# Performance work log

Measured on AMD Instinct MI355X. Metric: run time of the kernel, lower is better.

## Reference

```python
import jax, jax.numpy as jnp
import numpy as np
import math

B, S, D = 4, 4096, 2048
H = 16
DH = D // H  # 128
EPS = 1e-5


def _layer_norm(x, g, b):
    m = jnp.mean(x, axis=-1, keepdims=True)
    v = jnp.mean(jnp.square(x - m), axis=-1, keepdims=True)
    return (x - m) * jax.lax.rsqrt(v + EPS) * g + b


def setup_inputs() -> dict:
    key = jax.random.key(0)
    ks = jax.random.split(key, 12)
    s = 0.02
    return {
        "X": jax.random.normal(ks[0], (B, S, D), dtype=jnp.float32),
        "Wq": jax.random.normal(ks[1], (D, D), dtype=jnp.float32) * s,
        "bq": jnp.zeros((D,), dtype=jnp.float32),
        "Wk": jax.random.normal(ks[2], (D, D), dtype=jnp.float32) * s,
        "bk": jnp.zeros((D,), dtype=jnp.float32),
        "Wv": jax.random.normal(ks[3], (D, D), dtype=jnp.float32) * s,
        "bv": jnp.zeros((D,), dtype=jnp.float32),
        "g1": jnp.ones((D,), dtype=jnp.float32),
        "beta1": jnp.zeros((D,), dtype=jnp.float32),
        "W1": jax.random.normal(ks[4], (D, D), dtype=jnp.float32) * s,
        "b1": jnp.zeros((D,), dtype=jnp.float32),
        "W2": jax.random.normal(ks[5], (D, D), dtype=jnp.float32) * s,
        "b2": jnp.zeros((D,), dtype=jnp.float32),
        "g2": jnp.ones((D,), dtype=jnp.float32),
        "beta2": jnp.zeros((D,), dtype=jnp.float32),
    }


def reference(X, Wq, bq, Wk, bk, Wv, bv, g1, beta1, W1, b1, W2, b2, g2, beta2):
    # --- MultiHeadSelfAttention (faithful: .view, so attention is over HEADS per token) ---
    q = (X @ Wq + bq).reshape(B, S, H, DH)
    k = (X @ Wk + bk).reshape(B, S, H, DH)
    v = (X @ Wv + bv).reshape(B, S, H, DH)
    # [B, S, H, H] scores: heads attend to heads within the same position
    att = jnp.einsum('bshd,bstd->bsht', q, k) / math.sqrt(DH)
    att = jax.nn.softmax(att, axis=-1)
    y = jnp.einsum('bsht,bstd->bshd', att, v).reshape(B, S, D)
    # --- residual + LN1 ---
    X1 = _layer_norm(X + y, g1, beta1)
    # --- FeedForward: D -> D -> D with exact GELU ---
    h = jax.nn.gelu(X1 @ W1 + b1, approximate=False)
    y2 = h @ W2 + b2
    # --- residual + LN2 ---
    return _layer_norm(X1 + y2, g2, beta2)
```

## Files before the change

kernel.cpp:

```cpp
#include <hip/hip_runtime.h>
#include <math.h>

#define DM 2048
#define NT 16384
#define KD 2048
#define ND 2048

typedef __bf16 bf16x8 __attribute__((ext_vector_type(8)));
typedef float  f32x4  __attribute__((ext_vector_type(4)));

__device__ __forceinline__ void gld_lds16(const void* g, void* l) {
  __builtin_amdgcn_global_load_lds(
      (const __attribute__((address_space(1))) unsigned int*)g,
      (__attribute__((address_space(3))) unsigned int*)l, 16, 0, 0);
}

__global__ __launch_bounds__(256) void k_cast(const float* __restrict__ x,
                                              __bf16* __restrict__ y) {
  const size_t i = ((size_t)blockIdx.x * 256 + threadIdx.x) * 8;
  const float4 a = *(const float4*)(x + i);
  const float4 b = *(const float4*)(x + i + 4);
  bf16x8 o;
  o[0]=(__bf16)a.x; o[1]=(__bf16)a.y; o[2]=(__bf16)a.z; o[3]=(__bf16)a.w;
  o[4]=(__bf16)b.x; o[5]=(__bf16)b.y; o[6]=(__bf16)b.z; o[7]=(__bf16)b.w;
  *(bf16x8*)(y + i) = o;
}

__global__ __launch_bounds__(256) void k_transpose(const float* __restrict__ W,
                                                   __bf16* __restrict__ Wt) {
  __shared__ float t[32][33];
  const int tx = threadIdx.x, ty = threadIdx.y;
  const int n  = blockIdx.x * 32 + tx;
  const int k0 = blockIdx.y * 32;
  #pragma unroll
  for (int j = 0; j < 32; j += 8) t[ty + j][tx] = W[(size_t)(k0 + ty + j) * ND + n];
  __syncthreads();
  const int kk = k0 + tx;
  const int n0 = blockIdx.x * 32;
  #pragma unroll
  for (int j = 0; j < 32; j += 8)
    Wt[(size_t)(n0 + ty + j) * KD + kk] = (__bf16)t[tx][ty + j];
}

__global__ __launch_bounds__(256, 2) void k_gemm(
    const __bf16* __restrict__ A, const __bf16* __restrict__ Bt,
    const float* __restrict__ bias, const int mode,
    __bf16* __restrict__ outb, const float* __restrict__ resf,
    const __bf16* __restrict__ resb, float* __restrict__ outf) {
  __shared__ __bf16 As[128 * 32];
  __shared__ __bf16 Bs[128 * 32];
  const int tid  = threadIdx.x;
  const int wave = tid >> 6, lane = tid & 63;
  const int quad = lane >> 4, r16 = lane & 15;
  const int m0 = blockIdx.x * 128, n0 = blockIdx.y * 128;
  const int wm = (wave >> 1) * 64, wn = (wave & 1) * 64;

  const int srow = tid >> 2;
  const int scol = (tid & 3) * 8;
  const __bf16* Ap0 = A  + (size_t)(m0 + srow) * KD + scol;
  const __bf16* Ap1 = A  + (size_t)(m0 + 64 + srow) * KD + scol;
  const __bf16* Bp0 = Bt + (size_t)(n0 + srow) * KD + scol;
  const __bf16* Bp1 = Bt + (size_t)(n0 + 64 + srow) * KD + scol;
  __bf16* AsW0 = &As[wave * 512];
  __bf16* AsW1 = &As[2048 + wave * 512];
  __bf16* BsW0 = &Bs[wave * 512];
  __bf16* BsW1 = &Bs[2048 + wave * 512];

  f32x4 acc[4][4] = {};

  for (int k0 = 0; k0 < KD; k0 += 32) {
    gld_lds16(Ap0 + k0, AsW0);
    gld_lds16(Ap1 + k0, AsW1);
    gld_lds16(Bp0 + k0, BsW0);
    gld_lds16(Bp1 + k0, BsW1);
    __syncthreads();
    bf16x8 af[4], bfr[4];
    #pragma unroll
    for (int mi = 0; mi < 4; mi++)
      af[mi] = *(const bf16x8*)&As[(wm + mi * 16 + r16) * 32 + quad * 8];
    #pragma unroll
    for (int ni = 0; ni < 4; ni++)
      bfr[ni] = *(const bf16x8*)&Bs[(wn + ni * 16 + r16) * 32 + quad * 8];
    #pragma unroll
    for (int mi = 0; mi < 4; mi++)
      #pragma unroll
      for (int ni = 0; ni < 4; ni++)
        acc[mi][ni] = __builtin_amdgcn_mfma_f32_16x16x32_bf16(af[mi], bfr[ni], acc[mi][ni], 0, 0, 0);
    __syncthreads();
  }

  #pragma unroll
  for (int ni = 0; ni < 4; ni++) {
    const int gn = n0 + wn + ni * 16 + r16;
    const float bv = bias[gn];
    #pragma unroll
    for (int mi = 0; mi < 4; mi++) {
      const int gm = m0 + wm + mi * 16 + quad * 4;
      if (mode == 0) {
        #pragma unroll
        for (int r = 0; r < 4; r++)
          outb[(size_t)(gm + r) * ND + gn] = (__bf16)(acc[mi][ni][r] + bv);
      } else if (mode == 1) {
        #pragma unroll
        for (int r = 0; r < 4; r++) {
          float v = acc[mi][ni][r] + bv;
          float gel = 0.5f * v * (1.0f + erff(v * 0.70710678118654752f));
          outb[(size_t)(gm + r) * ND + gn] = (__bf16)gel;
        }
      } else if (mode == 2) {
        #pragma unroll
        for (int r = 0; r < 4; r++) {
          const size_t o = (size_t)(gm + r) * ND + gn;
          outf[o] = acc[mi][ni][r] + bv + resf[o];
        }
      } else {
        #pragma unroll
        for (int r = 0; r < 4; r++) {
          const size_t o = (size_t)(gm + r) * ND + gn;
          outf[o] = acc[mi][ni][r] + bv + (float)resb[o];
        }
      }
    }
  }
}

__global__ __launch_bounds__(256) void k_attn_ln1(
    const __bf16* __restrict__ Q, const __bf16* __restrict__ Kq,
    const __bf16* __restrict__ V, const float* __restrict__ X,
    const float* __restrict__ g1, const float* __restrict__ be1,
    float* __restrict__ X1, __bf16* __restrict__ X1b, const int use_f32) {
  __shared__ float qs[16 * 132];
  __shared__ float ks[16 * 132];
  __shared__ float vs[16 * 132];
  __shared__ float p[256];
  __shared__ float red[8];
  const int tid = threadIdx.x;
  const size_t base = (size_t)blockIdx.x * DM;
  const int e0 = tid * 8;

  {
    const int row = e0 >> 7, c0 = e0 & 127;
    bf16x8 qv = *(const bf16x8*)(Q + base + e0);
    bf16x8 kv = *(const bf16x8*)(Kq + base + e0);
    bf16x8 vv = *(const bf16x8*)(V + base + e0);
    #pragma unroll
    for (int j = 0; j < 8; j++) {
      qs[row * 132 + c0 + j] = (float)qv[j];
      ks[row * 132 + c0 + j] = (float)kv[j];
      vs[row * 132 + c0 + j] = (float)vv[j];
    }
  }
  __syncthreads();

  {
    const int h = tid >> 4, t = tid & 15;
    const float* qp = &qs[h * 132];
    const float* kp = &ks[t * 132];
    float s = 0.f;
    #pragma unroll
    for (int d = 0; d < 128; d++) s += qp[d] * kp[d];
    s *= 0.08838834764831845f;
    float mx = s;
    #pragma unroll
    for (int off = 8; off; off >>= 1) mx = fmaxf(mx, __shfl_xor(mx, off, 16));
    const float e = expf(s - mx);
    float sum = e;
    #pragma unroll
    for (int off = 8; off; off >>= 1) sum += __shfl_xor(sum, off, 16);
    p[tid] = e / sum;
  }
  __syncthreads();

  float zloc[8];
  float zs = 0.f, zq = 0.f;
  {
    const float4 x1 = *(const float4*)(X + base + e0);
    const float4 x2 = *(const float4*)(X + base + e0 + 4);
    const float xr[8] = {x1.x, x1.y, x1.z, x1.w, x2.x, x2.y, x2.z, x2.w};
    const int hh = e0 >> 7;
    const int d0 = e0 & 127;
    const float* pp = &p[hh * 16];
    #pragma unroll
    for (int j = 0; j < 8; j++) {
      float y = 0.f;
      #pragma unroll
      for (int t2 = 0; t2 < 16; t2++) y += pp[t2] * vs[t2 * 132 + d0 + j];
      const float z = xr[j] + y;
      zloc[j] = z; zs += z; zq += z * z;
    }
  }
  #pragma unroll
  for (int off = 32; off; off >>= 1) {
    zs += __shfl_xor(zs, off, 64);
    zq += __shfl_xor(zq, off, 64);
  }
  const int wave = tid >> 6, lane = tid & 63;
  if (lane == 0) { red[wave] = zs; red[4 + wave] = zq; }
  __syncthreads();
  zs = red[0] + red[1] + red[2] + red[3];
  zq = red[4] + red[5] + red[6] + red[7];
  const float mean = zs * (1.f / DM);
  const float var = zq * (1.f / DM) - mean * mean;
  const float rstd = rsqrtf(var + 1e-5f);
  {
    float o[8];
    #pragma unroll
    for (int j = 0; j < 8; j++)
      o[j] = (zloc[j] - mean) * rstd * g1[e0 + j] + be1[e0 + j];
    if (use_f32) {
      *(float4*)(X1 + base + e0)     = make_float4(o[0], o[1], o[2], o[3]);
      *(float4*)(X1 + base + e0 + 4) = make_float4(o[4], o[5], o[6], o[7]);
    }
    bf16x8 ob;
    #pragma unroll
    for (int j = 0; j < 8; j++) ob[j] = (__bf16)o[j];
    *(bf16x8*)(X1b + base + e0) = ob;
  }
}

__global__ __launch_bounds__(256) void k_ln2(const float* __restrict__ Z,
                                             const float* __restrict__ g,
                                             const float* __restrict__ be,
                                             float* __restrict__ out) {
  __shared__ float red[8];
  const int tid = threadIdx.x;
  const size_t base = (size_t)blockIdx.x * DM;
  const int e0 = tid * 8;
  const float4 a = *(const float4*)(Z + base + e0);
  const float4 b = *(const float4*)(Z + base + e0 + 4);
  float z[8] = {a.x, a.y, a.z, a.w, b.x, b.y, b.z, b.w};
  float zs = 0.f, zq = 0.f;
  #pragma unroll
  for (int j = 0; j < 8; j++) { zs += z[j]; zq += z[j] * z[j]; }
  #pragma unroll
  for (int off = 32; off; off >>= 1) {
    zs += __shfl_xor(zs, off, 64);
    zq += __shfl_xor(zq, off, 64);
  }
  const int wave = tid >> 6, lane = tid & 63;
  if (lane == 0) { red[wave] = zs; red[4 + wave] = zq; }
  __syncthreads();
  zs = red[0] + red[1] + red[2] + red[3];
  zq = red[4] + red[5] + red[6] + red[7];
  const float mean = zs * (1.f / DM);
  const float var = zq * (1.f / DM) - mean * mean;
  const float rstd = rsqrtf(var + 1e-5f);
  float o[8];
  #pragma unroll
  for (int j = 0; j < 8; j++)
    o[j] = (z[j] - mean) * rstd * g[e0 + j] + be[e0 + j];
  *(float4*)(out + base + e0)     = make_float4(o[0], o[1], o[2], o[3]);
  *(float4*)(out + base + e0 + 4) = make_float4(o[4], o[5], o[6], o[7]);
}

extern "C" void kernel_launch(void* const* d_in, const int* in_sizes, int n_in,
                              void* d_out, int out_size, void* d_ws, size_t ws_size,
                              hipStream_t stream) {
  const float* X   = (const float*)d_in[0];
  const float* Wq  = (const float*)d_in[1];
  const float* bq  = (const float*)d_in[2];
  const float* Wk  = (const float*)d_in[3];
  const float* bk  = (const float*)d_in[4];
  const float* Wv  = (const float*)d_in[5];
  const float* bv  = (const float*)d_in[6];
  const float* g1  = (const float*)d_in[7];
  const float* be1 = (const float*)d_in[8];
  const float* W1  = (const float*)d_in[9];
  const float* b1  = (const float*)d_in[10];
  const float* W2  = (const float*)d_in[11];
  const float* b2  = (const float*)d_in[12];
  const float* g2  = (const float*)d_in[13];
  const float* be2 = (const float*)d_in[14];
  float* out = (float*)d_out;

  char* ws = (char*)d_ws;
  size_t off = 0;
  auto alloc = [&](size_t b) -> char* {
    char* p = ws + off;
    off += (b + 255) & ~(size_t)255;
    return p;
  };
  const size_t EL = (size_t)NT * DM;
  __bf16* Xb  = (__bf16*)alloc(EL * 2);
  __bf16* Wqt = (__bf16*)alloc((size_t)ND * KD * 2);
  __bf16* Wkt = (__bf16*)alloc((size_t)ND * KD * 2);
  __bf16* Wvt = (__bf16*)alloc((size_t)ND * KD * 2);
  __bf16* W1t = (__bf16*)alloc((size_t)ND * KD * 2);
  __bf16* W2t = (__bf16*)alloc((size_t)ND * KD * 2);
  __bf16* Qb  = (__bf16*)alloc(EL * 2);
  __bf16* Kb  = (__bf16*)alloc(EL * 2);
  __bf16* Vb  = (__bf16*)alloc(EL * 2);
  __bf16* X1b = (__bf16*)alloc(EL * 2);
  const int use_f32 = (ws_size >= off + EL * 4) ? 1 : 0;
  float* X1 = nullptr;
  if (use_f32) X1 = (float*)alloc(EL * 4);
  __bf16* Hb = Xb;
  float*  Z  = (float*)Qb;

  k_cast<<<dim3(NT * DM / 2048), dim3(256), 0, stream>>>(X, Xb);
  dim3 tb(32, 8), tg(64, 64);
  k_transpose<<<tg, tb, 0, stream>>>(Wq, Wqt);
  k_transpose<<<tg, tb, 0, stream>>>(Wk, Wkt);
  k_transpose<<<tg, tb, 0, stream>>>(Wv, Wvt);
  k_transpose<<<tg, tb, 0, stream>>>(W1, W1t);
  k_transpose<<<tg, tb, 0, stream>>>(W2, W2t);
  dim3 gg(NT / 128, ND / 128);
  k_gemm<<<gg, dim3(256), 0, stream>>>(Xb, Wqt, bq, 0, Qb, nullptr, nullptr, nullptr);
  k_gemm<<<gg, dim3(256), 0, stream>>>(Xb, Wkt, bk, 0, Kb, nullptr, nullptr, nullptr);
  k_gemm<<<gg, dim3(256), 0, stream>>>(Xb, Wvt, bv, 0, Vb, nullptr, nullptr, nullptr);
  k_attn_ln1<<<dim3(NT), dim3(256), 0, stream>>>(Qb, Kb, Vb, X, g1, be1, X1, X1b, use_f32);
  k_gemm<<<gg, dim3(256), 0, stream>>>(X1b, W1t, b1, 1, Hb, nullptr, nullptr, nullptr);
  k_gemm<<<gg, dim3(256), 0, stream>>>(Hb, W2t, b2, use_f32 ? 2 : 3, nullptr, X1, X1b, Z);
  k_ln2<<<dim3(NT), dim3(256), 0, stream>>>(Z, g2, be2, out);
}
```

Baseline: 1.412 ms.

## Fuse QKV projections into one GEMM with LDS-staged vectorized epilogue

Concatenates the transposed Wq/Wk/Wv into one 6144-wide weight and the three biases into one buffer, so Q, K and V come from a single GEMM launch instead of three. The attention kernel reads an interleaved QKV row. The GEMM now uses a 1D grid with N-fastest tile ordering, which should improve reuse of A tiles in cache. The bf16-output epilogues stage results through LDS so each thread writes 16-byte vectors instead of scattered 2-byte stores. The costs are one extra small bias-copy kernel and a larger QKV workspace buffer.

```diff
diff --git a/kernel.cpp b/kernel.cpp
--- a/kernel.cpp
+++ b/kernel.cpp
@@ -4,7 +4,6 @@
 #define DM 2048
 #define NT 16384
 #define KD 2048
-#define ND 2048
 
 typedef __bf16 bf16x8 __attribute__((ext_vector_type(8)));
 typedef float  f32x4  __attribute__((ext_vector_type(4)));
@@ -33,7 +32,7 @@
   const int n  = blockIdx.x * 32 + tx;
   const int k0 = blockIdx.y * 32;
   #pragma unroll
-  for (int j = 0; j < 32; j += 8) t[ty + j][tx] = W[(size_t)(k0 + ty + j) * ND + n];
+  for (int j = 0; j < 32; j += 8) t[ty + j][tx] = W[(size_t)(k0 + ty + j) * DM + n];
   __syncthreads();
   const int kk = k0 + tx;
   const int n0 = blockIdx.x * 32;
@@ -42,9 +41,18 @@
     Wt[(size_t)(n0 + ty + j) * KD + kk] = (__bf16)t[tx][ty + j];
 }
 
+__global__ __launch_bounds__(256) void k_bias3(const float* __restrict__ a,
+                                               const float* __restrict__ b,
+                                               const float* __restrict__ c,
+                                               float* __restrict__ o) {
+  const int i = blockIdx.x * 256 + threadIdx.x;
+  o[i] = (i < 2048) ? a[i] : ((i < 4096) ? b[i - 2048] : c[i - 4096]);
+}
+
 __global__ __launch_bounds__(256, 2) void k_gemm(
     const __bf16* __restrict__ A, const __bf16* __restrict__ Bt,
-    const float* __restrict__ bias, const int mode,
+    const float* __restrict__ bias, const int mode, const int ntile_n,
+    const int NS,
     __bf16* __restrict__ outb, const float* __restrict__ resf,
     const __bf16* __restrict__ resb, float* __restrict__ outf) {
   __shared__ __bf16 As[128 * 32];
@@ -52,7 +60,9 @@
   const int tid  = threadIdx.x;
   const int wave = tid >> 6, lane = tid & 63;
   const int quad = lane >> 4, r16 = lane & 15;
-  const int m0 = blockIdx.x * 128, n0 = blockIdx.y * 128;
+  const int bid = blockIdx.x;
+  const int m0 = (bid / ntile_n) * 128;
+  const int n0 = (bid % ntile_n) * 128;
   const int wm = (wave >> 1) * 64, wn = (wave & 1) * 64;
 
   const int srow = tid >> 2;
@@ -89,44 +99,61 @@
     __syncthreads();
   }
 
-  #pragma unroll
-  for (int ni = 0; ni < 4; ni++) {
-    const int gn = n0 + wn + ni * 16 + r16;
-    const float bv = bias[gn];
-    #pragma unroll
-    for (int mi = 0; mi < 4; mi++) {
-      const int gm = m0 + wm + mi * 16 + quad * 4;
-      if (mode == 0) {
+  if (mode <= 1) {
+    __bf16* eb = (wave < 2) ? &As[wave * 2048] : &Bs[(wave - 2) * 2048];
+    #pragma unroll
+    for (int half = 0; half < 2; half++) {
+      #pragma unroll
+      for (int nj = 0; nj < 2; nj++) {
+        const int ni = half * 2 + nj;
+        const int gn = n0 + wn + ni * 16 + r16;
+        const float bv = bias[gn];
         #pragma unroll
-        for (int r = 0; r < 4; r++)
-          outb[(size_t)(gm + r) * ND + gn] = (__bf16)(acc[mi][ni][r] + bv);
-      } else if (mode == 1) {
-        #pragma unroll
-        for (int r = 0; r < 4; r++) {
-          float v = acc[mi][ni][r] + bv;
-          float gel = 0.5f * v * (1.0f + erff(v * 0.70710678118654752f));
-          outb[(size_t)(gm + r) * ND + gn] = (__bf16)gel;
-        }
-      } else if (mode == 2) {
-        #pragma unroll
-        for (int r = 0; r < 4; r++) {
-          const size_t o = (size_t)(gm + r) * ND + gn;
-          outf[o] = acc[mi][ni][r] + bv + resf[o];
-        }
-      } else {
-        #pragma unroll
-        for (int r = 0; r < 4; r++) {
-          const size_t o = (size_t)(gm + r) * ND + gn;
-          outf[o] = acc[mi][ni][r] + bv + (float)resb[o];
+        for (int mi = 0; mi < 4; mi++) {
+          #pragma unroll
+          for (int r = 0; r < 4; r++) {
+            float v = acc[mi][ni][r] + bv;
+            if (mode == 1) v = 0.5f * v * (1.0f + erff(v * 0.70710678118654752f));
+            eb[(mi * 16 + quad * 4 + r) * 32 + nj * 16 + r16] = (__bf16)v;
+          }
         }
       }
+      #pragma unroll
+      for (int rd = 0; rd < 4; rd++) {
+        const int row = rd * 16 + (lane >> 2);
+        const int c0 = (lane & 3) * 8;
+        bf16x8 vv = *(const bf16x8*)&eb[row * 32 + c0];
+        *(bf16x8*)(outb + (size_t)(m0 + wm + row) * NS + n0 + wn + half * 32 + c0) = vv;
+      }
+    }
+  } else {
+    #pragma unroll
+    for (int ni = 0; ni < 4; ni++) {
+      const int gn = n0 + wn + ni * 16 + r16;
+      const float bv = bias[gn];
+      #pragma unroll
+      for (int mi = 0; mi < 4; mi++) {
+        const int gm = m0 + wm + mi * 16 + quad * 4;
+        if (mode == 2) {
+          #pragma unroll
+          for (int r = 0; r < 4; r++) {
+            const size_t o = (size_t)(gm + r) * NS + gn;
+            outf[o] = acc[mi][ni][r] + bv + resf[o];
+          }
+        } else {
+          #pragma unroll
+          for (int r = 0; r < 4; r++) {
+            const size_t o = (size_t)(gm + r) * NS + gn;
+            outf[o] = acc[mi][ni][r] + bv + (float)resb[o];
+          }
+        }
+      }
     }
   }
 }
 
 __global__ __launch_bounds__(256) void k_attn_ln1(
-    const __bf16* __restrict__ Q, const __bf16* __restrict__ Kq,
-    const __bf16* __restrict__ V, const float* __restrict__ X,
+    const __bf16* __restrict__ QKV, const float* __restrict__ X,
     const float* __restrict__ g1, const float* __restrict__ be1,
     float* __restrict__ X1, __bf16* __restrict__ X1b, const int use_f32) {
   __shared__ float qs[16 * 132];
@@ -135,14 +162,15 @@
   __shared__ float p[256];
   __shared__ float red[8];
   const int tid = threadIdx.x;
-  const size_t base = (size_t)blockIdx.x * DM;
+  const size_t qbase = (size_t)blockIdx.x * 6144;
+  const size_t base  = (size_t)blockIdx.x * DM;
   const int e0 = tid * 8;
 
   {
     const int row = e0 >> 7, c0 = e0 & 127;
-    bf16x8 qv = *(const bf16x8*)(Q + base + e0);
-    bf16x8 kv = *(const bf16x8*)(Kq + base + e0);
-    bf16x8 vv = *(const bf16x8*)(V + base + e0);
+    bf16x8 qv = *(const bf16x8*)(QKV + qbase + e0);
+    bf16x8 kv = *(const bf16x8*)(QKV + qbase + 2048 + e0);
+    bf16x8 vv = *(const bf16x8*)(QKV + qbase + 4096 + e0);
     #pragma unroll
     for (int j = 0; j < 8; j++) {
       qs[row * 132 + c0 + j] = (float)qv[j];
@@ -280,36 +308,36 @@
     off += (b + 255) & ~(size_t)255;
     return p;
   };
-  const size_t EL = (size_t)NT * DM;
-  __bf16* Xb  = (__bf16*)alloc(EL * 2);
-  __bf16* Wqt = (__bf16*)alloc((size_t)ND * KD * 2);
-  __bf16* Wkt = (__bf16*)alloc((size_t)ND * KD * 2);
-  __bf16* Wvt = (__bf16*)alloc((size_t)ND * KD * 2);
-  __bf16* W1t = (__bf16*)alloc((size_t)ND * KD * 2);
-  __bf16* W2t = (__bf16*)alloc((size_t)ND * KD * 2);
-  __bf16* Qb  = (__bf16*)alloc(EL * 2);
-  __bf16* Kb  = (__bf16*)alloc(EL * 2);
-  __bf16* Vb  = (__bf16*)alloc(EL * 2);
-  __bf16* X1b = (__bf16*)alloc(EL * 2);
+  const size_t EL  = (size_t)NT * DM;
+  const size_t EL3 = (size_t)NT * 6144;
+  __bf16* Xb    = (__bf16*)alloc(EL * 2);
+  __bf16* Wqkvt = (__bf16*)alloc((size_t)6144 * KD * 2);
+  __bf16* W1t   = (__bf16*)alloc((size_t)DM * KD * 2);
+  __bf16* W2t   = (__bf16*)alloc((size_t)DM * KD * 2);
+  float*  b3    = (float*)alloc(6144 * 4);
+  __bf16* QKVb  = (__bf16*)alloc(EL3 * 2);
+  __bf16* X1b   = (__bf16*)alloc(EL * 2);
   const int use_f32 = (ws_size >= off + EL * 4) ? 1 : 0;
   float* X1 = nullptr;
   if (use_f32) X1 = (float*)alloc(EL * 4);
   __bf16* Hb = Xb;
-  float*  Z  = (float*)Qb;
+  float*  Z  = (float*)QKVb;
 
   k_cast<<<dim3(NT * DM / 2048), dim3(256), 0, stream>>>(X, Xb);
   dim3 tb(32, 8), tg(64, 64);
-  k_transpose<<<tg, tb, 0, stream>>>(Wq, Wqt);
-  k_transpose<<<tg, tb, 0, stream>>>(Wk, Wkt);
-  k_transpose<<<tg, tb, 0, stream>>>(Wv, Wvt);
+  k_transpose<<<tg, tb, 0, stream>>>(Wq, Wqkvt);
+  k_transpose<<<tg, tb, 0, stream>>>(Wk, Wqkvt + (size_t)2048 * KD);
+  k_transpose<<<tg, tb, 0, stream>>>(Wv, Wqkvt + (size_t)4096 * KD);
   k_transpose<<<tg, tb, 0, stream>>>(W1, W1t);
   k_transpose<<<tg, tb, 0, stream>>>(W2, W2t);
-  dim3 gg(NT / 128, ND / 128);
-  k_gemm<<<gg, dim3(256), 0, stream>>>(Xb, Wqt, bq, 0, Qb, nullptr, nullptr, nullptr);
-  k_gemm<<<gg, dim3(256), 0, stream>>>(Xb, Wkt, bk, 0, Kb, nullptr, nullptr, nullptr);
-  k_gemm<<<gg, dim3(256), 0, stream>>>(Xb, Wvt, bv, 0, Vb, nullptr, nullptr, nullptr);
-  k_attn_ln1<<<dim3(NT), dim3(256), 0, stream>>>(Qb, Kb, Vb, X, g1, be1, X1, X1b, use_f32);
-  k_gemm<<<gg, dim3(256), 0, stream>>>(X1b, W1t, b1, 1, Hb, nullptr, nullptr, nullptr);
-  k_gemm<<<gg, dim3(256), 0, stream>>>(Hb, W2t, b2, use_f32 ? 2 : 3, nullptr, X1, X1b, Z);
+  k_bias3<<<dim3(24), dim3(256), 0, stream>>>(bq, bk, bv, b3);
+
+  k_gemm<<<dim3((NT / 128) * 48), dim3(256), 0, stream>>>(
+      Xb, Wqkvt, b3, 0, 48, 6144, QKVb, nullptr, nullptr, nullptr);
+  k_attn_ln1<<<dim3(NT), dim3(256), 0, stream>>>(QKVb, X, g1, be1, X1, X1b, use_f32);
+  k_gemm<<<dim3((NT / 128) * 16), dim3(256), 0, stream>>>(
+      X1b, W1t, b1, 1, 16, 2048, Hb, nullptr, nullptr, nullptr);
+  k_gemm<<<dim3((NT / 128) * 16), dim3(256), 0, stream>>>(
+      Hb, W2t, b2, use_f32 ? 2 : 3, 16, 2048, nullptr, X1, X1b, Z);
   k_ln2<<<dim3(NT), dim3(256), 0, stream>>>(Z, g2, be2, out);
 }
```

New measurement: 1.382 ms. 1.02x faster.
